# Kernel optimization log

Measured on AMD Instinct MI355X. Metric: run time of the kernel, lower is better.

The kernel has to match this reference:

```python
import jax, jax.numpy as jnp
import numpy as np

EPS = 1e-6

def setup_inputs() -> dict:
    key = jax.random.key(0)
    ks = jax.random.split(key, 7)
    T, B, S, A, D = 512, 32, 64, 8, 32
    x = jax.random.normal(ks[0], (T, B, D), dtype=jnp.float32)
    a = jax.random.normal(ks[1], (T, B, A), dtype=jnp.float32)
    mask = jnp.ones((T, B), dtype=jnp.float32)
    mu = jax.random.normal(ks[2], (S, D), dtype=jnp.float32)
    logv = 0.1 * jax.random.normal(ks[3], (S, D), dtype=jnp.float32)
    init_logits = jax.random.normal(ks[4], (S,), dtype=jnp.float32)
    w_base = 0.1 * jax.random.normal(ks[5], (S, S), dtype=jnp.float32)
    w_act = 0.1 * jax.random.normal(ks[6], (A, S, S), dtype=jnp.float32)
    return {"x": x, "a": a, "mask": mask, "mu": mu, "logv": logv,
            "init_logits": init_logits, "w_base": w_base, "w_act": w_act}

def reference(x, a, mask, mu, logv, init_logits, w_base, w_act):
    T, B, D = x.shape
    S = mu.shape[0]
    # Gaussian (diag) emission log-likelihood for every state: [T, B, S]
    var = jnp.exp(logv)
    diff = x[:, :, None, :] - mu  # [T, B, S, D]
    logp_x = -0.5 * jnp.sum(diff * diff / var + logv + jnp.log(2.0 * jnp.pi), axis=-1)
    # Logistic (action-conditioned) transition matrices for t=1..T-1: [T-1, B, S, S]
    trans = jax.nn.softmax(w_base + jnp.einsum('tba,aij->tbij', a[:-1], w_act), axis=-1)
    logp0 = jax.nn.log_softmax(init_logits)
    # alpha_0
    alpha0 = jax.nn.softmax(logp_x[0] + logp0, axis=-1)

    def fwd_step(b, inp):
        tr, lx = inp
        logp_z = jnp.log(jnp.sum(tr * b[:, :, None] + EPS, axis=-2))
        b_new = jax.nn.softmax(lx + logp_z, axis=-1)
        return b_new, b_new

    _, alpha_rest = jax.lax.scan(fwd_step, alpha0, (trans, logp_x[1:]))
    alpha = jnp.concatenate([alpha0[None], alpha_rest], axis=0)  # [T, B, S]

    log_trans = jnp.log(trans + EPS)

    def bwd_step(logb, inp):
        ltr, lx, m = inp
        new = jax.scipy.special.logsumexp(lx[:, None, :] + ltr + logb[:, None, :], axis=-1)
        new = new * (m[:, None] == 1)
        return new, new

    _, lb = jax.lax.scan(bwd_step, jnp.zeros((B, S), x.dtype),
                         (log_trans, logp_x[1:], mask[1:]), reverse=True)
    log_beta = jnp.concatenate([lb, jnp.zeros((1, B, S), x.dtype)], axis=0)  # [T, B, S]

    # Posterior state marginals
    q_z = jax.nn.softmax(jnp.log(alpha + EPS) + log_beta, axis=-1)
    return q_z
```

## Files before the change

kernel.cpp:

```cpp
#include <hip/hip_runtime.h>
#include <math.h>

#define TT 512
#define BB 32
#define SS 64
#define AA 8
#define DD 32
#define EPSF 1e-6f
#define SEPS (64.0f * 1e-6f)
#define TS 68

__device__ __forceinline__ int   f2i(float x){ return __float_as_int(x); }
__device__ __forceinline__ float i2f(int x){ return __int_as_float(x); }
__device__ __forceinline__ float readlane_f(float v, int l){
  return i2f(__builtin_amdgcn_readlane(f2i(v), l));
}
template<int CTRL, int RMASK>
__device__ __forceinline__ float dpp_add(float x){
  return x + i2f(__builtin_amdgcn_update_dpp(0, f2i(x), CTRL, RMASK, 0xf, true));
}
__device__ __forceinline__ float wave_sum_dpp(float x){
  x = dpp_add<0x111, 0xf>(x);
  x = dpp_add<0x112, 0xf>(x);
  x = dpp_add<0x114, 0xf>(x);
  x = dpp_add<0x118, 0xf>(x);
  x = dpp_add<0x142, 0xa>(x);
  x = dpp_add<0x143, 0xc>(x);
  return readlane_f(x, 63);
}
__device__ __forceinline__ float wave_sum(float v){
  #pragma unroll
  for (int m = 1; m < 64; m <<= 1) v += __shfl_xor(v, m, 64);
  return v;
}
__device__ __forceinline__ float wave_max(float v){
  #pragma unroll
  for (int m = 1; m < 64; m <<= 1) v = fmaxf(v, __shfl_xor(v, m, 64));
  return v;
}
#define BARRIER() asm volatile("s_waitcnt lgkmcnt(0)\n\ts_barrier" ::: "memory")

__global__ void prep_kernel(const float* __restrict__ logv,
                            float* __restrict__ iv, float* __restrict__ cs){
  int gid = blockIdx.x * blockDim.x + threadIdx.x;
  if (gid < SS * DD) iv[gid] = __expf(-logv[gid]);
  if (gid < SS){
    float s = 0.f;
    #pragma unroll
    for (int d = 0; d < DD; ++d) s += logv[gid * DD + d];
    cs[gid] = s + (float)DD * 1.8378770664093453f;
  }
}

__global__ __launch_bounds__(256) void logpx_kernel(
    const float* __restrict__ x, const float* __restrict__ mu,
    const float* __restrict__ iv, const float* __restrict__ cs,
    float* __restrict__ slx_out){
  const int lane = threadIdx.x & 63;
  const int w = threadIdx.x >> 6;
  const int row = blockIdx.x * 4 + w;
  const float* __restrict__ xp  = x  + row * DD;
  const float* __restrict__ mup = mu + lane * DD;
  const float* __restrict__ ivp = iv + lane * DD;
  float acc = 0.f;
  #pragma unroll
  for (int d = 0; d < DD; ++d){
    float diff = xp[d] - mup[d];
    acc = fmaf(diff * diff, ivp[d], acc);
  }
  float lx = -0.5f * (acc + cs[lane]);
  float mx = wave_max(lx);
  slx_out[row * SS + lane] = lx - mx;
}

__global__ __launch_bounds__(768) void scan_kernel(
    const float* __restrict__ slx, const float* __restrict__ mask,
    const float* __restrict__ il, const float* __restrict__ a,
    const float* __restrict__ w_base, const float* __restrict__ w_act,
    float* __restrict__ alpha, float* __restrict__ log_beta){
  const int lane = threadIdx.x & 63;
  const int w    = threadIdx.x >> 6;
  const bool is_fwd = (blockIdx.x < BB);
  const int b = is_fwd ? blockIdx.x : (blockIdx.x - BB);

  __shared__ __align__(16) float tile[3][SS * TS];
  __shared__ float rsp[3][8][SS];
  __shared__ float fpart[2][4][SS];
  __shared__ __align__(16) float aLDS[TT * AA];
  __shared__ float mLDS[TT];

  for (int idx = threadIdx.x; idx < TT * AA; idx += 768){
    int t = idx >> 3, k = idx & 7;
    aLDS[idx] = a[(t * BB + b) * AA + k];
  }
  for (int idx = threadIdx.x; idx < TT; idx += 768)
    mLDS[idx] = mask[idx * BB + b];

  if (w >= 4){
    const int pw = w - 4;
    const int jb = pw * 8;
    float wb[8], wa[8][8];
    #pragma unroll
    for (int jj = 0; jj < 8; ++jj){
      wb[jj] = w_base[lane * SS + jb + jj];
      #pragma unroll
      for (int k = 0; k < 8; ++k)
        wa[k][jj] = w_act[(k * SS + lane) * SS + jb + jj];
    }
    float aa[8], aan[8];
    {
      const int t0 = is_fwd ? 0 : (TT - 2);
      const float* __restrict__ ap = a + (t0 * BB + b) * AA;
      #pragma unroll
      for (int k = 0; k < 8; ++k) aa[k] = ap[k];
      const int t1 = is_fwd ? 1 : (TT - 3);
      const float* __restrict__ ap1 = a + (t1 * BB + b) * AA;
      #pragma unroll
      for (int k = 0; k < 8; ++k) aan[k] = ap1[k];
    }
    {
      float ev[8]; float racc = 0.f;
      #pragma unroll
      for (int jj = 0; jj < 8; ++jj){
        float u = wb[jj];
        #pragma unroll
        for (int k = 0; k < 8; ++k) u = fmaf(aa[k], wa[k][jj], u);
        ev[jj] = __expf(u); racc += ev[jj];
      }
      *(float4*)&tile[0][lane * TS + jb]     = make_float4(ev[0],ev[1],ev[2],ev[3]);
      *(float4*)&tile[0][lane * TS + jb + 4] = make_float4(ev[4],ev[5],ev[6],ev[7]);
      rsp[0][pw][lane] = racc;
    }
    BARRIER();
    int tw = 1;
    for (int s = 0; s < TT - 1; ++s){
      if (s <= TT - 3){
        #pragma unroll
        for (int k = 0; k < 8; ++k) aa[k] = aan[k];
        if (s + 1 <= TT - 3){
          const int tn = is_fwd ? (s + 2) : (TT - 4 - s);
          #pragma unroll
          for (int k = 0; k < 8; ++k) aan[k] = aLDS[tn * AA + k];
        }
        float ev[8]; float racc = 0.f;
        #pragma unroll
        for (int jj = 0; jj < 8; ++jj){
          float u = wb[jj];
          #pragma unroll
          for (int k = 0; k < 8; ++k) u = fmaf(aa[k], wa[k][jj], u);
          ev[jj] = __expf(u); racc += ev[jj];
        }
        *(float4*)&tile[tw][lane * TS + jb]     = make_float4(ev[0],ev[1],ev[2],ev[3]);
        *(float4*)&tile[tw][lane * TS + jb + 4] = make_float4(ev[4],ev[5],ev[6],ev[7]);
        rsp[tw][pw][lane] = racc;
        tw = (tw == 2) ? 0 : tw + 1;
      }
      BARRIER();
    }
  } else if (is_fwd){
    const int wb16 = __builtin_amdgcn_readfirstlane(w * 16);
    float u = __expf(slx[b * SS + lane] + il[lane]);
    float c = __builtin_amdgcn_rcpf(wave_sum_dpp(u));
    if (w == 0) alpha[b * SS + lane] = u * c;
    float slxn = slx[(BB + b) * SS + lane];
    float elxc = 0.f;
    BARRIER();
    int ts = 0;
    for (int s = 0; s < TT - 1; ++s){
      if (s > 0){
        const int fs = (s - 1) & 1;
        float S = (fpart[fs][0][lane] + fpart[fs][1][lane])
                + (fpart[fs][2][lane] + fpart[fs][3][lane]);
        u = elxc * fmaf(c, S, SEPS);
        c = __builtin_amdgcn_rcpf(wave_sum_dpp(u));
        if (w == 0) alpha[(s * BB + b) * SS + lane] = u * c;
      }
      float rs = ((rsp[ts][0][lane] + rsp[ts][1][lane]) + (rsp[ts][2][lane] + rsp[ts][3][lane]))
               + ((rsp[ts][4][lane] + rsp[ts][5][lane]) + (rsp[ts][6][lane] + rsp[ts][7][lane]));
      float va = u * __builtin_amdgcn_rcpf(rs);
      const float* __restrict__ tp = &tile[ts][0];
      float a0 = 0.f, a1 = 0.f, a2 = 0.f, a3 = 0.f;
      #pragma unroll
      for (int r = 0; r < 16; r += 4){
        a0 = fmaf(readlane_f(va, wb16 + r    ), tp[(wb16 + r    ) * TS + lane], a0);
        a1 = fmaf(readlane_f(va, wb16 + r + 1), tp[(wb16 + r + 1) * TS + lane], a1);
        a2 = fmaf(readlane_f(va, wb16 + r + 2), tp[(wb16 + r + 2) * TS + lane], a2);
        a3 = fmaf(readlane_f(va, wb16 + r + 3), tp[(wb16 + r + 3) * TS + lane], a3);
      }
      fpart[s & 1][w][lane] = (a0 + a1) + (a2 + a3);
      elxc = __expf(slxn);
      if (s + 2 <= TT - 1) slxn = slx[((s + 2) * BB + b) * SS + lane];
      ts = (ts == 2) ? 0 : ts + 1;
      BARRIER();
    }
    {
      const int fs = (TT - 2) & 1;
      float S = (fpart[fs][0][lane] + fpart[fs][1][lane])
              + (fpart[fs][2][lane] + fpart[fs][3][lane]);
      u = elxc * fmaf(c, S, SEPS);
      c = __builtin_amdgcn_rcpf(wave_sum_dpp(u));
      if (w == 0) alpha[((TT - 1) * BB + b) * SS + lane] = u * c;
    }
  } else {
    const int wb16 = __builtin_amdgcn_readfirstlane(w * 16);
    float breg = 0.f, rWc = 1.f;
    if (w == 0) log_beta[((TT - 1) * BB + b) * SS + lane] = 0.f;
    float slxc = slx[((TT - 1) * BB + b) * SS + lane];
    float mprev = 1.f;
    BARRIER();
    int ts = 0, pts = 2;
    for (int s = 0; s < TT - 1; ++s){
      if (s > 0){
        const int fs = (s - 1) & 1;
        float eh = (fpart[fs][0][lane] + fpart[fs][1][lane])
                 + (fpart[fs][2][lane] + fpart[fs][3][lane]);
        float rsv = ((rsp[pts][0][lane] + rsp[pts][1][lane]) + (rsp[pts][2][lane] + rsp[pts][3][lane]))
                  + ((rsp[pts][4][lane] + rsp[pts][5][lane]) + (rsp[pts][6][lane] + rsp[pts][7][lane]));
        float v = __logf(fmaf(eh * __builtin_amdgcn_rcpf(rsv), rWc, EPSF));
        breg = (mprev == 1.0f) ? v : 0.0f;
        if (w == 0) log_beta[((TT - 1 - s) * BB + b) * SS + lane] = breg;
      }
      float wgt = __expf(slxc + breg);
      float W = wave_sum_dpp(wgt);
      rWc = __builtin_amdgcn_rcpf(W);
      const float* __restrict__ tp = &tile[ts][lane * TS + wb16];
      float4 e0 = *(const float4*)(tp);
      float4 e1 = *(const float4*)(tp + 4);
      float4 e2 = *(const float4*)(tp + 8);
      float4 e3 = *(const float4*)(tp + 12);
      float a0 = 0.f, a1 = 0.f, a2 = 0.f, a3 = 0.f;
      a0 = fmaf(readlane_f(wgt, wb16 + 0),  e0.x, a0);
      a1 = fmaf(readlane_f(wgt, wb16 + 1),  e0.y, a1);
      a2 = fmaf(readlane_f(wgt, wb16 + 2),  e0.z, a2);
      a3 = fmaf(readlane_f(wgt, wb16 + 3),  e0.w, a3);
      a0 = fmaf(readlane_f(wgt, wb16 + 4),  e1.x, a0);
      a1 = fmaf(readlane_f(wgt, wb16 + 5),  e1.y, a1);
      a2 = fmaf(readlane_f(wgt, wb16 + 6),  e1.z, a2);
      a3 = fmaf(readlane_f(wgt, wb16 + 7),  e1.w, a3);
      a0 = fmaf(readlane_f(wgt, wb16 + 8),  e2.x, a0);
      a1 = fmaf(readlane_f(wgt, wb16 + 9),  e2.y, a1);
      a2 = fmaf(readlane_f(wgt, wb16 + 10), e2.z, a2);
      a3 = fmaf(readlane_f(wgt, wb16 + 11), e2.w, a3);
      a0 = fmaf(readlane_f(wgt, wb16 + 12), e3.x, a0);
      a1 = fmaf(readlane_f(wgt, wb16 + 13), e3.y, a1);
      a2 = fmaf(readlane_f(wgt, wb16 + 14), e3.z, a2);
      a3 = fmaf(readlane_f(wgt, wb16 + 15), e3.w, a3);
      fpart[s & 1][w][lane] = (a0 + a1) + (a2 + a3);
      mprev = mLDS[TT - 1 - s];
      if (s <= TT - 3) slxc = slx[((TT - 2 - s) * BB + b) * SS + lane];
      pts = ts; ts = (ts == 2) ? 0 : ts + 1;
      BARRIER();
    }
    {
      const int fs = (TT - 2) & 1;
      float eh = (fpart[fs][0][lane] + fpart[fs][1][lane])
               + (fpart[fs][2][lane] + fpart[fs][3][lane]);
      float rsv = ((rsp[pts][0][lane] + rsp[pts][1][lane]) + (rsp[pts][2][lane] + rsp[pts][3][lane]))
                + ((rsp[pts][4][lane] + rsp[pts][5][lane]) + (rsp[pts][6][lane] + rsp[pts][7][lane]));
      float v = __logf(fmaf(eh * __builtin_amdgcn_rcpf(rsv), rWc, EPSF));
      breg = (mprev == 1.0f) ? v : 0.0f;
      if (w == 0) log_beta[b * SS + lane] = breg;
    }
  }
}

__global__ __launch_bounds__(256) void qz_kernel(
    const float* __restrict__ alpha, const float* __restrict__ log_beta,
    float* __restrict__ out){
  const int lane = threadIdx.x & 63;
  const int w = threadIdx.x >> 6;
  const int row = blockIdx.x * 4 + w;
  float v = __logf(alpha[row * SS + lane] + EPSF) + log_beta[row * SS + lane];
  float mx = wave_max(v);
  float e = __expf(v - mx);
  float sm = wave_sum(e);
  out[row * SS + lane] = e * __builtin_amdgcn_rcpf(sm);
}

extern "C" void kernel_launch(void* const* d_in, const int* in_sizes, int n_in,
                              void* d_out, int out_size, void* d_ws, size_t ws_size,
                              hipStream_t stream){
  const float* x      = (const float*)d_in[0];
  const float* a      = (const float*)d_in[1];
  const float* mask   = (const float*)d_in[2];
  const float* mu     = (const float*)d_in[3];
  const float* logv   = (const float*)d_in[4];
  const float* il     = (const float*)d_in[5];
  const float* w_base = (const float*)d_in[6];
  const float* w_act  = (const float*)d_in[7];
  float* out = (float*)d_out;

  float* ws = (float*)d_ws;
  const size_t TBS = (size_t)TT * BB * SS;
  float* iv       = ws;
  float* cs       = ws + 2048;
  float* slx      = ws + 4096;
  float* alpha    = slx + TBS;
  float* log_beta = alpha + TBS;

  prep_kernel<<<8, 256, 0, stream>>>(logv, iv, cs);
  logpx_kernel<<<TT * BB / 4, 256, 0, stream>>>(x, mu, iv, cs, slx);
  scan_kernel<<<2 * BB, 768, 0, stream>>>(slx, mask, il, a, w_base, w_act,
                                          alpha, log_beta);
  qz_kernel<<<TT * BB / 4, 256, 0, stream>>>(alpha, log_beta, out);
}
```

Before: 402.5 us.

## Precompute transition matrices in windows and run single-wave scans from global memory

Splits the fused scan kernel into two parts. A produce_kernel materializes softmax transition matrices for a window of timesteps into workspace, with a transposed layout for the forward pass. A lightweight 64-thread scan_win_kernel then streams those matrices with register double-buffering, and the host loops over windows with state carried between launches. This takes the matrix softmax off the serial critical path and spreads it across the GPU. The cost is heavy global memory traffic (about 16 KB per step per batch), many kernel launches, and reliance on workspace size; it falls back to the old kernel when the workspace is too small.

```diff
diff --git a/kernel.cpp b/kernel.cpp
--- a/kernel.cpp
+++ b/kernel.cpp
@@ -73,6 +73,183 @@
   slx_out[row * SS + lane] = lx - mx;
 }
 
+__global__ __launch_bounds__(256) void produce_kernel(
+    const float* __restrict__ a, const float* __restrict__ w_base,
+    const float* __restrict__ w_act, float* __restrict__ ET,
+    float* __restrict__ E, int f_lo, int f_cnt, int b_lo, int b_cnt){
+  const int lane = threadIdx.x & 63;
+  const int wv = threadIdx.x >> 6;
+  const int jb = wv * 16;
+  int blk = blockIdx.x;
+  const bool isF = blk < f_cnt * 8;
+  if (!isF) blk -= f_cnt * 8;
+  const int rel = blk >> 3;
+  const int b0 = (blk & 7) * 4;
+  const int t = (isF ? f_lo : b_lo) + rel;
+
+  float4 wb4[4], wa4[8][4];
+  {
+    const float4* wbp = (const float4*)(w_base + lane * SS + jb);
+    #pragma unroll
+    for (int q = 0; q < 4; ++q) wb4[q] = wbp[q];
+    #pragma unroll
+    for (int k = 0; k < 8; ++k){
+      const float4* wap = (const float4*)(w_act + ((k * SS + lane) * SS) + jb);
+      #pragma unroll
+      for (int q = 0; q < 4; ++q) wa4[k][q] = wap[q];
+    }
+  }
+  __shared__ float part[4][4][SS];
+  #pragma unroll
+  for (int g = 0; g < 4; ++g){
+    const int b = b0 + g;
+    float aa[8];
+    const float* __restrict__ ap = a + (t * BB + b) * AA;
+    #pragma unroll
+    for (int k = 0; k < 8; ++k) aa[k] = ap[k];
+    float4 uv[4];
+    #pragma unroll
+    for (int q = 0; q < 4; ++q){
+      uv[q] = wb4[q];
+      #pragma unroll
+      for (int k = 0; k < 8; ++k){
+        uv[q].x = fmaf(aa[k], wa4[k][q].x, uv[q].x);
+        uv[q].y = fmaf(aa[k], wa4[k][q].y, uv[q].y);
+        uv[q].z = fmaf(aa[k], wa4[k][q].z, uv[q].z);
+        uv[q].w = fmaf(aa[k], wa4[k][q].w, uv[q].w);
+      }
+    }
+    float ev[16]; float rpart = 0.f;
+    #pragma unroll
+    for (int q = 0; q < 4; ++q){
+      ev[4*q+0] = __expf(uv[q].x); ev[4*q+1] = __expf(uv[q].y);
+      ev[4*q+2] = __expf(uv[q].z); ev[4*q+3] = __expf(uv[q].w);
+      rpart += ev[4*q+0] + ev[4*q+1] + ev[4*q+2] + ev[4*q+3];
+    }
+    part[g][wv][lane] = rpart;
+    __syncthreads();
+    float rs = part[g][0][lane] + part[g][1][lane]
+             + part[g][2][lane] + part[g][3][lane];
+    float rn = __builtin_amdgcn_rcpf(rs);
+    const size_t tb = (size_t)(rel * BB + b) << 12;
+    if (isF){
+      float* __restrict__ dst = ET + tb;
+      #pragma unroll
+      for (int c = 0; c < 16; ++c) dst[(jb + c) * SS + lane] = ev[c] * rn;
+    } else {
+      float* __restrict__ dst = E + tb;
+      #pragma unroll
+      for (int q = 0; q < 4; ++q){
+        *(float4*)&dst[lane * SS + jb + 4*q] =
+          make_float4(ev[4*q]*rn, ev[4*q+1]*rn, ev[4*q+2]*rn, ev[4*q+3]*rn);
+      }
+    }
+  }
+}
+
+__global__ __launch_bounds__(64, 1) void scan_win_kernel(
+    const float* __restrict__ slx, const float* __restrict__ mask,
+    const float* __restrict__ il,
+    const float* __restrict__ ET, const float* __restrict__ E,
+    float* __restrict__ alpha, float* __restrict__ log_beta,
+    float* __restrict__ fwd_u, float* __restrict__ bwd_b,
+    int f_lo, int f_cnt, int b_lo, int b_cnt){
+  const int lane = threadIdx.x;
+  if (blockIdx.x < BB){
+    const int b = blockIdx.x;
+    float u, c;
+    if (f_lo == 0){
+      u = __expf(slx[b * SS + lane] + il[lane]);
+      c = __builtin_amdgcn_rcpf(wave_sum_dpp(u));
+      alpha[b * SS + lane] = u * c;
+    } else {
+      u = fwd_u[b * SS + lane];
+      c = __builtin_amdgcn_rcpf(wave_sum_dpp(u));
+    }
+    float4 eA[16], eB[16]; float slA, slB;
+    int r = 0;
+    {
+      const float4* rp = (const float4*)ET + ((size_t)(0 * BB + b) << 10) + lane * 16;
+      #pragma unroll
+      for (int q = 0; q < 16; ++q) eA[q] = rp[q];
+      slA = slx[(f_lo + 1) * (BB * SS) + b * SS + lane];
+    }
+    auto fstep = [&](float4 (&cur)[16], float4 (&nxt)[16], float& slc, float& sln){
+      const int rn = (r + 1 < f_cnt) ? r + 1 : r;
+      const float4* np = (const float4*)ET + ((size_t)(rn * BB + b) << 10) + lane * 16;
+      #pragma unroll
+      for (int q = 0; q < 16; ++q) nxt[q] = np[q];
+      int tn = f_lo + 2 + r; if (tn > TT - 1) tn = TT - 1;
+      sln = slx[tn * (BB * SS) + b * SS + lane];
+      float a0 = 0.f, a1 = 0.f, a2 = 0.f, a3 = 0.f;
+      #pragma unroll
+      for (int q = 0; q < 16; ++q){
+        a0 = fmaf(readlane_f(u, 4*q + 0), cur[q].x, a0);
+        a1 = fmaf(readlane_f(u, 4*q + 1), cur[q].y, a1);
+        a2 = fmaf(readlane_f(u, 4*q + 2), cur[q].z, a2);
+        a3 = fmaf(readlane_f(u, 4*q + 3), cur[q].w, a3);
+      }
+      float S = (a0 + a1) + (a2 + a3);
+      u = __expf(slc) * fmaf(c, S, SEPS);
+      c = __builtin_amdgcn_rcpf(wave_sum_dpp(u));
+      alpha[(f_lo + 1 + r) * (BB * SS) + b * SS + lane] = u * c;
+      ++r;
+    };
+    for (;;){
+      fstep(eA, eB, slA, slB); if (r >= f_cnt) break;
+      fstep(eB, eA, slB, slA); if (r >= f_cnt) break;
+    }
+    fwd_u[b * SS + lane] = u;
+  } else {
+    const int bb = blockIdx.x - BB;
+    float breg;
+    if (b_lo + b_cnt == TT - 1){
+      breg = 0.f;
+      log_beta[(TT - 1) * (BB * SS) + bb * SS + lane] = 0.f;
+    } else {
+      breg = bwd_b[bb * SS + lane];
+    }
+    float4 eA[16], eB[16]; float slA, slB, mA, mB;
+    int r = b_cnt - 1;
+    {
+      const float4* rp = (const float4*)E + ((size_t)(r * BB + bb) << 10) + lane * 16;
+      #pragma unroll
+      for (int q = 0; q < 16; ++q) eA[q] = rp[q];
+      slA = slx[(b_lo + r + 1) * (BB * SS) + bb * SS + lane];
+      mA  = mask[(b_lo + r + 1) * BB + bb];
+    }
+    auto bstep = [&](float4 (&cur)[16], float4 (&nxt)[16],
+                     float& slc, float& sln, float& mc, float& mn){
+      const int rn = (r - 1 >= 0) ? r - 1 : 0;
+      const float4* np = (const float4*)E + ((size_t)(rn * BB + bb) << 10) + lane * 16;
+      #pragma unroll
+      for (int q = 0; q < 16; ++q) nxt[q] = np[q];
+      sln = slx[(b_lo + rn + 1) * (BB * SS) + bb * SS + lane];
+      mn  = mask[(b_lo + rn + 1) * BB + bb];
+      float wgt = __expf(slc + breg);
+      float W = wave_sum_dpp(wgt);
+      float rW = __builtin_amdgcn_rcpf(W);
+      float a0 = 0.f, a1 = 0.f, a2 = 0.f, a3 = 0.f;
+      #pragma unroll
+      for (int q = 0; q < 16; ++q){
+        a0 = fmaf(readlane_f(wgt, 4*q + 0), cur[q].x, a0);
+        a1 = fmaf(readlane_f(wgt, 4*q + 1), cur[q].y, a1);
+        a2 = fmaf(readlane_f(wgt, 4*q + 2), cur[q].z, a2);
+        a3 = fmaf(readlane_f(wgt, 4*q + 3), cur[q].w, a3);
+      }
+      float v = __logf(fmaf((a0 + a1) + (a2 + a3), rW, EPSF));
+      breg = (mc == 1.0f) ? v : 0.0f;
+      log_beta[(b_lo + r) * (BB * SS) + bb * SS + lane] = breg;
+      --r;
+    };
+    for (;;){
+      bstep(eA, eB, slA, slB, mA, mB); if (r < 0) break;
+      bstep(eB, eA, slB, slA, mB, mA); if (r < 0) break;
+    }
+    bwd_b[bb * SS + lane] = breg;
+  }
+}
+
 __global__ __launch_bounds__(768) void scan_kernel(
     const float* __restrict__ slx, const float* __restrict__ mask,
     const float* __restrict__ il, const float* __restrict__ a,
@@ -82,20 +259,17 @@
   const int w    = threadIdx.x >> 6;
   const bool is_fwd = (blockIdx.x < BB);
   const int b = is_fwd ? blockIdx.x : (blockIdx.x - BB);
-
   __shared__ __align__(16) float tile[3][SS * TS];
   __shared__ float rsp[3][8][SS];
   __shared__ float fpart[2][4][SS];
   __shared__ __align__(16) float aLDS[TT * AA];
   __shared__ float mLDS[TT];
-
   for (int idx = threadIdx.x; idx < TT * AA; idx += 768){
     int t = idx >> 3, k = idx & 7;
     aLDS[idx] = a[(t * BB + b) * AA + k];
   }
   for (int idx = threadIdx.x; idx < TT; idx += 768)
     mLDS[idx] = mask[idx * BB + b];
-
   if (w >= 4){
     const int pw = w - 4;
     const int jb = pw * 8;
@@ -297,10 +471,38 @@
   float* slx      = ws + 4096;
   float* alpha    = slx + TBS;
   float* log_beta = alpha + TBS;
+  float* fwd_u    = log_beta + TBS;
+  float* bwd_b    = fwd_u + 2048;
+  const size_t base = 4096 + 3 * TBS + 8192;
+  float* ET = ws + base;
+
+  const size_t avail = (ws_size / 4 > base) ? (ws_size / 4 - base) : 0;
+  int W = 0;
+  const int tiers[5] = {128, 64, 32, 16, 8};
+  for (int i = 0; i < 5; ++i){
+    if ((size_t)tiers[i] * 2 * BB * 4096 <= avail){ W = tiers[i]; break; }
+  }
 
   prep_kernel<<<8, 256, 0, stream>>>(logv, iv, cs);
   logpx_kernel<<<TT * BB / 4, 256, 0, stream>>>(x, mu, iv, cs, slx);
-  scan_kernel<<<2 * BB, 768, 0, stream>>>(slx, mask, il, a, w_base, w_act,
-                                          alpha, log_beta);
+  if (W > 0){
+    float* E = ET + (size_t)W * BB * 4096;
+    const int nw = (TT - 1 + W - 1) / W;
+    for (int k = 0; k < nw; ++k){
+      const int f_lo = k * W;
+      const int f_cnt = ((TT - 1) - f_lo < W) ? ((TT - 1) - f_lo) : W;
+      const int b_hi = (TT - 1) - k * W;
+      const int b_lo = (b_hi - W > 0) ? (b_hi - W) : 0;
+      const int b_cnt = b_hi - b_lo;
+      produce_kernel<<<f_cnt * 8 + b_cnt * 8, 256, 0, stream>>>(
+          a, w_base, w_act, ET, E, f_lo, f_cnt, b_lo, b_cnt);
+      scan_win_kernel<<<2 * BB, 64, 0, stream>>>(
+          slx, mask, il, ET, E, alpha, log_beta, fwd_u, bwd_b,
+          f_lo, f_cnt, b_lo, b_cnt);
+    }
+  } else {
+    scan_kernel<<<2 * BB, 768, 0, stream>>>(slx, mask, il, a, w_base, w_act,
+                                            alpha, log_beta);
+  }
   qz_kernel<<<TT * BB / 4, 256, 0, stream>>>(alpha, log_beta, out);
 }
```

Measured after the change: 941.3 us. +133.9%, slower.
